# Performance work log

Measured on AMD Instinct MI355X. Metric: run time of the kernel, lower is better.

The kernel has to match this reference:

```python
import jax, jax.numpy as jnp
import numpy as np

DIM = 512
HEADS = 8
HEAD_DIM = DIM // HEADS
FFN = 1536
WIN = 16
EPS = 1e-6


def rms_norm(x, w):
    var = jnp.mean(x * x, axis=-1, keepdims=True)
    return x * jax.lax.rsqrt(var + EPS) * w


def rotate_half(x):
    x1, x2 = jnp.split(x, 2, axis=-1)
    return jnp.concatenate([-x2, x1], axis=-1)


def apply_rope(q, k, inv_freq, position_ids):
    # q,k: [B,H,S,D]; inv_freq: [D//2]; position_ids: [B,S]
    ang = position_ids[:, :, None].astype(jnp.float32) * inv_freq[None, None, :]  # [B,S,D/2]
    cos = jnp.concatenate([jnp.cos(ang), jnp.cos(ang)], axis=-1)[:, None]  # [B,1,S,D]
    sin = jnp.concatenate([jnp.sin(ang), jnp.sin(ang)], axis=-1)[:, None]
    q = q * cos + rotate_half(q) * sin
    k = k * cos + rotate_half(k) * sin
    return q, k


def setup_inputs() -> dict:
    key = jax.random.key(0)
    ks = jax.random.split(key, 12)
    B, S = 2, 4096
    x = jax.random.normal(ks[0], (B, S, DIM), dtype=jnp.float32)
    inv_freq = 1.0 / (10000.0 ** (jnp.arange(0, HEAD_DIM, 2, dtype=jnp.float32) / HEAD_DIM))  # [D/2]
    position_ids = jnp.broadcast_to(jnp.arange(S, dtype=jnp.int64), (B, S))
    key_padding_mask = jnp.zeros((B, S), dtype=bool)  # True = padded (ignored)
    s = 0.02
    return {
        "x": x,
        "rope_freqs": inv_freq,
        "position_ids": position_ids,
        "key_padding_mask": key_padding_mask,
        "norm1_w": jnp.ones((DIM,), jnp.float32),
        "wq": jax.random.normal(ks[1], (DIM, DIM), jnp.float32) * s,
        "wk": jax.random.normal(ks[2], (DIM, DIM), jnp.float32) * s,
        "wv": jax.random.normal(ks[3], (DIM, DIM), jnp.float32) * s,
        "wo": jax.random.normal(ks[4], (DIM, DIM), jnp.float32) * s,
        "norm2_w": jnp.ones((DIM,), jnp.float32),
        "w1": jax.random.normal(ks[5], (DIM, FFN), jnp.float32) * s,  # gate proj
        "w2": jax.random.normal(ks[6], (DIM, FFN), jnp.float32) * s,  # up proj
        "w3": jax.random.normal(ks[7], (FFN, DIM), jnp.float32) * s,  # down proj
    }


def local_attention(h, rope_freqs, position_ids, key_padding_mask, wq, wk, wv, wo):
    B, S, _ = h.shape
    q = jnp.einsum("bsd,de->bse", h, wq).reshape(B, S, HEADS, HEAD_DIM).transpose(0, 2, 1, 3)
    k = jnp.einsum("bsd,de->bse", h, wk).reshape(B, S, HEADS, HEAD_DIM).transpose(0, 2, 1, 3)
    v = jnp.einsum("bsd,de->bse", h, wv).reshape(B, S, HEADS, HEAD_DIM).transpose(0, 2, 1, 3)
    q, k = apply_rope(q, k, rope_freqs, position_ids)

    offs = jnp.arange(-WIN, WIN + 1)                       # [W]
    pos = jnp.arange(S)[:, None] + offs[None, :]           # [S,W]
    in_range = (pos >= 0) & (pos < S)                      # [S,W]
    pos_c = jnp.clip(pos, 0, S - 1)
    k_band = k[:, :, pos_c]                                # [B,H,S,W,D]
    v_band = v[:, :, pos_c]
    scores = jnp.einsum("bhsd,bhswd->bhsw", q, k_band) * (HEAD_DIM ** -0.5)
    keep = in_range[None, None] & (~key_padding_mask[:, pos_c])[:, None]  # [B,1->H,S,W]
    scores = jnp.where(keep, scores, -1e9)
    attn = jax.nn.softmax(scores, axis=-1)
    out = jnp.einsum("bhsw,bhswd->bhsd", attn, v_band)
    out = out.transpose(0, 2, 1, 3).reshape(B, S, DIM)
    return jnp.einsum("bsd,de->bse", out, wo)


def swiglu(h, w1, w2, w3):
    return jnp.einsum("bsf,fd->bsd", jax.nn.silu(h @ w1) * (h @ w2), w3)


def reference(x, rope_freqs, position_ids, key_padding_mask,
              norm1_w, wq, wk, wv, wo, norm2_w, w1, w2, w3):
    x = x + local_attention(rms_norm(x, norm1_w), rope_freqs, position_ids,
                            key_padding_mask, wq, wk, wv, wo)
    x = x + swiglu(rms_norm(x, norm2_w), w1, w2, w3)
    return x
```

## Files before the change

kernel.cpp:

```cpp
#include <hip/hip_runtime.h>
#include <math.h>

#define DIM   512
#define HEADS 8
#define HD    64
#define FFN_N 1536
#define WIN   16
#define SEQ   4096
#define BAND  (64 + 2 * WIN)
#define LDH   72

#define QKVN  1536

typedef __attribute__((ext_vector_type(8))) short bf16x8;
typedef __attribute__((ext_vector_type(4))) float f32x4;
typedef _Float16 f16;
typedef __attribute__((ext_vector_type(2))) _Float16 f16x2;

__device__ inline unsigned short f2bf(float f) {
  union { float f; unsigned u; } v; v.f = f;
  unsigned r = (v.u + 0x7FFF + ((v.u >> 16) & 1)) >> 16;
  return (unsigned short)r;
}

__device__ __forceinline__ float fast_rcp(float x) {
#if __has_builtin(__builtin_amdgcn_rcpf)
  return __builtin_amdgcn_rcpf(x);
#else
  return 1.0f / x;
#endif
}

__device__ __forceinline__ void gl2lds16(const void* g, void* l) {
  __builtin_amdgcn_global_load_lds(
      (const __attribute__((address_space(1))) unsigned int*)g,
      (__attribute__((address_space(3))) unsigned int*)l, 16, 0, 0);
}

__global__ __launch_bounds__(256) void k_preamble(
    const float* __restrict__ wq, const float* __restrict__ wk, const float* __restrict__ wv,
    const float* __restrict__ wo, const float* __restrict__ w1, const float* __restrict__ w2,
    const float* __restrict__ w3,
    unsigned short* __restrict__ BTqkv, unsigned short* __restrict__ BTwo,
    unsigned short* __restrict__ BTw12, unsigned short* __restrict__ BTw3,
    const float* __restrict__ invf, float* __restrict__ Ct, float* __restrict__ St,
    const float* __restrict__ X, const float* __restrict__ n1w,
    unsigned short* __restrict__ H, int ntok) {
  int bid = blockIdx.x;
  if (bid < 3328) {
    const float* src; unsigned short* dst; int K, N, t;
    if      (bid < 256)  { src = wq; dst = BTqkv;               K = 512;  N = 512;  t = bid; }
    else if (bid < 512)  { src = wk; dst = BTqkv + 512 * 512;   K = 512;  N = 512;  t = bid - 256; }
    else if (bid < 768)  { src = wv; dst = BTqkv + 1024 * 512;  K = 512;  N = 512;  t = bid - 512; }
    else if (bid < 1024) { src = wo; dst = BTwo;                K = 512;  N = 512;  t = bid - 768; }
    else if (bid < 1792) { src = w1; dst = BTw12;               K = 512;  N = 1536; t = bid - 1024; }
    else if (bid < 2560) { src = w2; dst = BTw12 + 1536 * 512;  K = 512;  N = 1536; t = bid - 1792; }
    else                 { src = w3; dst = BTw3;                K = 1536; N = 512;  t = bid - 2560; }
    int ntn = N >> 5;
    int tn = t % ntn, tk = t / ntn;
    __shared__ float T[32][33];
    int r = threadIdx.x >> 3, c = (threadIdx.x & 7) << 2;
    float4 s = *(const float4*)(src + (size_t)(tk * 32 + r) * N + tn * 32 + c);
    T[r][c + 0] = s.x; T[r][c + 1] = s.y; T[r][c + 2] = s.z; T[r][c + 3] = s.w;
    __syncthreads();
    ushort4 o = make_ushort4(f2bf(T[c + 0][r]), f2bf(T[c + 1][r]), f2bf(T[c + 2][r]), f2bf(T[c + 3][r]));
    *(ushort4*)(dst + (size_t)(tn * 32 + r) * K + tk * 32 + c) = o;
  } else if (bid < 3840) {
    int idx = (bid - 3328) * 256 + threadIdx.x;
    int p = idx & 31;
    int s = idx >> 5;
    float ang = (float)s * invf[p];
    float sn, cs;
    __sincosf(ang, &sn, &cs);
    Ct[idx] = cs;
    St[idx] = sn;
  } else {
    int wave = (bid - 3840) * 4 + (threadIdx.x >> 6);
    if (wave >= ntok) return;
    int lane = threadIdx.x & 63;
    const float* x = X + (size_t)wave * DIM;
    float4 a = *(const float4*)(x + lane * 4);
    float4 b = *(const float4*)(x + 256 + lane * 4);
    float ss = a.x*a.x + a.y*a.y + a.z*a.z + a.w*a.w
             + b.x*b.x + b.y*b.y + b.z*b.z + b.w*b.w;
#pragma unroll
    for (int off = 32; off; off >>= 1) ss += __shfl_xor(ss, off, 64);
    float r = rsqrtf(ss * (1.0f / DIM) + 1e-6f);
    float4 wa = *(const float4*)(n1w + lane * 4);
    float4 wb = *(const float4*)(n1w + 256 + lane * 4);
    unsigned short* o = H + (size_t)wave * DIM;
    *(ushort4*)(o + lane * 4)       = make_ushort4(f2bf(a.x*r*wa.x), f2bf(a.y*r*wa.y), f2bf(a.z*r*wa.z), f2bf(a.w*r*wa.w));
    *(ushort4*)(o + 256 + lane * 4) = make_ushort4(f2bf(b.x*r*wb.x), f2bf(b.y*r*wb.y), f2bf(b.z*r*wb.z), f2bf(b.w*r*wb.w));
  }
}

__global__ __launch_bounds__(256) void k_rmsnorm(const float* __restrict__ X,
                                                 const float* __restrict__ W,
                                                 unsigned short* __restrict__ O, int ntok) {
  int wave = blockIdx.x * 4 + (threadIdx.x >> 6);
  if (wave >= ntok) return;
  int lane = threadIdx.x & 63;
  const float* x = X + (size_t)wave * DIM;
  float4 a = *(const float4*)(x + lane * 4);
  float4 b = *(const float4*)(x + 256 + lane * 4);
  float ss = a.x*a.x + a.y*a.y + a.z*a.z + a.w*a.w
           + b.x*b.x + b.y*b.y + b.z*b.z + b.w*b.w;
#pragma unroll
  for (int off = 32; off; off >>= 1) ss += __shfl_xor(ss, off, 64);
  float r = rsqrtf(ss * (1.0f / DIM) + 1e-6f);
  float4 wa = *(const float4*)(W + lane * 4);
  float4 wb = *(const float4*)(W + 256 + lane * 4);
  unsigned short* o = O + (size_t)wave * DIM;
  *(ushort4*)(o + lane * 4)       = make_ushort4(f2bf(a.x*r*wa.x), f2bf(a.y*r*wa.y), f2bf(a.z*r*wa.z), f2bf(a.w*r*wa.w));
  *(ushort4*)(o + 256 + lane * 4) = make_ushort4(f2bf(b.x*r*wb.x), f2bf(b.y*r*wb.y), f2bf(b.z*r*wb.z), f2bf(b.w*r*wb.w));
}

__global__ __launch_bounds__(256) void k_mgemm(
    const unsigned short* __restrict__ A, const unsigned short* __restrict__ BT,
    float* __restrict__ C, const float* __restrict__ R, int M, int N, int K) {
  __shared__ __align__(16) unsigned short As[128 * 32];
  __shared__ __align__(16) unsigned short Bs[64 * 32];
  int tid = threadIdx.x;
  int lane = tid & 63, wave = tid >> 6;
  int q4 = lane >> 4, l16 = lane & 15;
  int bN = blockIdx.x, bM = blockIdx.y;

  f32x4 acc[2][4];
#pragma unroll
  for (int i = 0; i < 2; ++i)
#pragma unroll
    for (int j = 0; j < 4; ++j) acc[i][j] = (f32x4){0.f, 0.f, 0.f, 0.f};

  int lrow = lane >> 2;
  int cg   = (((lane & 3) ^ ((lane >> 3) & 3)) << 3);
  unsigned short* AsW0 = As + (wave * 32) * 32;
  unsigned short* AsW1 = As + (wave * 32 + 16) * 32;
  unsigned short* BsW  = Bs + (wave * 16) * 32;
  const unsigned short* Ag0 = A  + (size_t)(bM * 128 + wave * 32 + lrow) * K + cg;
  const unsigned short* Ag1 = Ag0 + (size_t)16 * K;
  const unsigned short* Bg  = BT + (size_t)(bN * 64 + wave * 16 + lrow) * K + cg;

  int xc = ((q4 ^ ((l16 >> 1) & 3)) << 3);

  for (int k0 = 0; k0 < K; k0 += 32) {
    __syncthreads();
    gl2lds16(Ag0 + k0, AsW0);
    gl2lds16(Ag1 + k0, AsW1);
    gl2lds16(Bg  + k0, BsW);
    __syncthreads();
    bf16x8 af[2], bf[4];
#pragma unroll
    for (int mi = 0; mi < 2; ++mi)
      af[mi] = *(const bf16x8*)&As[(wave * 32 + mi * 16 + l16) * 32 + xc];
#pragma unroll
    for (int ni = 0; ni < 4; ++ni)
      bf[ni] = *(const bf16x8*)&Bs[(ni * 16 + l16) * 32 + xc];
#pragma unroll
    for (int mi = 0; mi < 2; ++mi)
#pragma unroll
      for (int ni = 0; ni < 4; ++ni)
        acc[mi][ni] = __builtin_amdgcn_mfma_f32_16x16x32_bf16(af[mi], bf[ni], acc[mi][ni], 0, 0, 0);
  }
#pragma unroll
  for (int mi = 0; mi < 2; ++mi)
#pragma unroll
    for (int ni = 0; ni < 4; ++ni) {
      int col = bN * 64 + ni * 16 + l16;
#pragma unroll
      for (int r = 0; r < 4; ++r) {
        int row = bM * 128 + wave * 32 + mi * 16 + q4 * 4 + r;
        float v = acc[mi][ni][r];
        if (R) v += R[(size_t)row * N + col];
        C[(size_t)row * N + col] = v;
      }
    }
}

__global__ __launch_bounds__(256) void k_mgemm128(
    const unsigned short* __restrict__ A, const unsigned short* __restrict__ BT,
    float* __restrict__ C, int M, int N, int K) {
  __shared__ __align__(16) unsigned short As[128 * 32];
  __shared__ __align__(16) unsigned short Bs[128 * 32];
  int tid = threadIdx.x;
  int lane = tid & 63, wave = tid >> 6;
  int wm = wave & 1, wn = wave >> 1;
  int q4 = lane >> 4, l16 = lane & 15;
  int bN = blockIdx.x, bM = blockIdx.y;

  f32x4 acc[4][4];
#pragma unroll
  for (int i = 0; i < 4; ++i)
#pragma unroll
    for (int j = 0; j < 4; ++j) acc[i][j] = (f32x4){0.f, 0.f, 0.f, 0.f};

  int lrow = lane >> 2;
  int cg   = (((lane & 3) ^ ((lane >> 3) & 3)) << 3);
  unsigned short* AsW0 = As + (wave * 32) * 32;
  unsigned short* AsW1 = As + (wave * 32 + 16) * 32;
  unsigned short* BsW0 = Bs + (wave * 32) * 32;
  unsigned short* BsW1 = Bs + (wave * 32 + 16) * 32;
  const unsigned short* Ag0 = A  + (size_t)(bM * 128 + wave * 32 + lrow) * K + cg;
  const unsigned short* Ag1 = Ag0 + (size_t)16 * K;
  const unsigned short* Bg0 = BT + (size_t)(bN * 128 + wave * 32 + lrow) * K + cg;
  const unsigned short* Bg1 = Bg0 + (size_t)16 * K;

  int xc = ((q4 ^ ((l16 >> 1) & 3)) << 3);

  for (int k0 = 0; k0 < K; k0 += 32) {
    __syncthreads();
    gl2lds16(Ag0 + k0, AsW0);
    gl2lds16(Ag1 + k0, AsW1);
    gl2lds16(Bg0 + k0, BsW0);
    gl2lds16(Bg1 + k0, BsW1);
    __syncthreads();
    bf16x8 af[4], bf[4];
#pragma unroll
    for (int mi = 0; mi < 4; ++mi)
      af[mi] = *(const bf16x8*)&As[(wm * 64 + mi * 16 + l16) * 32 + xc];
#pragma unroll
    for (int ni = 0; ni < 4; ++ni)
      bf[ni] = *(const bf16x8*)&Bs[(wn * 64 + ni * 16 + l16) * 32 + xc];
#pragma unroll
    for (int mi = 0; mi < 4; ++mi)
#pragma unroll
      for (int ni = 0; ni < 4; ++ni)
        acc[mi][ni] = __builtin_amdgcn_mfma_f32_16x16x32_bf16(af[mi], bf[ni], acc[mi][ni], 0, 0, 0);
  }
#pragma unroll
  for (int mi = 0; mi < 4; ++mi)
#pragma unroll
    for (int ni = 0; ni < 4; ++ni) {
      int col = bN * 128 + wn * 64 + ni * 16 + l16;
#pragma unroll
      for (int r = 0; r < 4; ++r) {
        int row = bM * 128 + wm * 64 + mi * 16 + q4 * 4 + r;
        C[(size_t)row * N + col] = acc[mi][ni][r];
      }
    }
}

__global__ __launch_bounds__(256) void k_mgemm_swiglu(
    const unsigned short* __restrict__ A, const unsigned short* __restrict__ B1T,
    const unsigned short* __restrict__ B2T, unsigned short* __restrict__ Y,
    int M, int N, int K) {
  __shared__ __align__(16) unsigned short As[128 * 32];
  __shared__ __align__(16) unsigned short B1s[64 * 32];
  __shared__ __align__(16) unsigned short B2s[64 * 32];
  int tid = threadIdx.x;
  int lane = tid & 63, wave = tid >> 6;
  int q4 = lane >> 4, l16 = lane & 15;
  int bN = blockIdx.x, bM = blockIdx.y;

  f32x4 acc[2][2][4];
#pragma unroll
  for (int t = 0; t < 2; ++t)
#pragma unroll
    for (int i = 0; i < 2; ++i)
#pragma unroll
      for (int j = 0; j < 4; ++j) acc[t][i][j] = (f32x4){0.f, 0.f, 0.f, 0.f};

  int lrow = lane >> 2;
  int cg   = (((lane & 3) ^ ((lane >> 3) & 3)) << 3);
  unsigned short* AsW0 = As  + (wave * 32) * 32;
  unsigned short* AsW1 = As  + (wave * 32 + 16) * 32;
  unsigned short* B1sW = B1s + (wave * 16) * 32;
  unsigned short* B2sW = B2s + (wave * 16) * 32;
  const unsigned short* Ag0 = A   + (size_t)(bM * 128 + wave * 32 + lrow) * K + cg;
  const unsigned short* Ag1 = Ag0 + (size_t)16 * K;
  const unsigned short* B1g = B1T + (size_t)(bN * 64 + wave * 16 + lrow) * K + cg;
  const unsigned short* B2g = B2T + (size_t)(bN * 64 + wave * 16 + lrow) * K + cg;

  int xc = ((q4 ^ ((l16 >> 1) & 3)) << 3);

  for (int k0 = 0; k0 < K; k0 += 32) {
    __syncthreads();
    gl2lds16(Ag0 + k0, AsW0);
    gl2lds16(Ag1 + k0, AsW1);
    gl2lds16(B1g + k0, B1sW);
    gl2lds16(B2g + k0, B2sW);
    __syncthreads();
    bf16x8 af[2], b1f[4], b2f[4];
#pragma unroll
    for (int mi = 0; mi < 2; ++mi)
      af[mi] = *(const bf16x8*)&As[(wave * 32 + mi * 16 + l16) * 32 + xc];
#pragma unroll
    for (int ni = 0; ni < 4; ++ni) {
      b1f[ni] = *(const bf16x8*)&B1s[(ni * 16 + l16) * 32 + xc];
      b2f[ni] = *(const bf16x8*)&B2s[(ni * 16 + l16) * 32 + xc];
    }
#pragma unroll
    for (int mi = 0; mi < 2; ++mi)
#pragma unroll
      for (int ni = 0; ni < 4; ++ni) {
        acc[0][mi][ni] = __builtin_amdgcn_mfma_f32_16x16x32_bf16(af[mi], b1f[ni], acc[0][mi][ni], 0, 0, 0);
        acc[1][mi][ni] = __builtin_amdgcn_mfma_f32_16x16x32_bf16(af[mi], b2f[ni], acc[1][mi][ni], 0, 0, 0);
      }
  }
#pragma unroll
  for (int mi = 0; mi < 2; ++mi)
#pragma unroll
    for (int ni = 0; ni < 4; ++ni) {
      int col = bN * 64 + ni * 16 + l16;
#pragma unroll
      for (int r = 0; r < 4; ++r) {
        int row = bM * 128 + wave * 32 + mi * 16 + q4 * 4 + r;
        float g = acc[0][mi][ni][r];
        float u = acc[1][mi][ni][r];
        float yv = g * fast_rcp(1.0f + __expf(-g)) * u;
        Y[(size_t)row * N + col] = f2bf(yv);
      }
    }
}

__global__ __launch_bounds__(128) void k_attn(const float* __restrict__ QKV,
                                              const float* __restrict__ Ct,
                                              const float* __restrict__ St,
                                              unsigned short* __restrict__ O) {
  __shared__ __align__(16) unsigned short KV[BAND * LDH];
  int tid = threadIdx.x;
  int c0 = blockIdx.x * 64;
  int h = blockIdx.y, b = blockIdx.z;

#pragma unroll
  for (int base = 0; base < BAND; base += 16) {
    int r  = base + (tid >> 3);
    int c8 = (tid & 7) << 3;
    int sr = c0 - WIN + r;
    int scl = min(max(sr, 0), SEQ - 1);
    const float* kr = QKV + ((size_t)(b * SEQ + scl)) * QKVN + h * HD + 512;
    int p = c8 & 31;
    float4 v0 = *(const float4*)(kr + c8);
    float4 v1 = *(const float4*)(kr + c8 + 4);
    float4 u0 = *(const float4*)(kr + (c8 ^ 32));
    float4 u1 = *(const float4*)(kr + (c8 ^ 32) + 4);
    float4 cv0 = *(const float4*)(Ct + scl * 32 + p);
    float4 cv1 = *(const float4*)(Ct + scl * 32 + p + 4);
    float4 sv0 = *(const float4*)(St + scl * 32 + p);
    float4 sv1 = *(const float4*)(St + scl * 32 + p + 4);
    float sg = (c8 < 32) ? -1.f : 1.f;
    union { int4 w; f16 x[8]; } pk;
    pk.x[0] = (f16)(v0.x * cv0.x + sg * u0.x * sv0.x);
    pk.x[1] = (f16)(v0.y * cv0.y + sg * u0.y * sv0.y);
    pk.x[2] = (f16)(v0.z * cv0.z + sg * u0.z * sv0.z);
    pk.x[3] = (f16)(v0.w * cv0.w + sg * u0.w * sv0.w);
    pk.x[4] = (f16)(v1.x * cv1.x + sg * u1.x * sv1.x);
    pk.x[5] = (f16)(v1.y * cv1.y + sg * u1.y * sv1.y);
    pk.x[6] = (f16)(v1.z * cv1.z + sg * u1.z * sv1.z);
    pk.x[7] = (f16)(v1.w * cv1.w + sg * u1.w * sv1.w);
    *(int4*)&KV[r * LDH + c8] = pk.w;
  }
  __syncthreads();

  int lane = tid & 63;
  int ql   = (tid >> 6) * 32 + (lane >> 1);
  int half = lane & 1;
  int s    = c0 + ql;

  const float* qp = QKV + ((size_t)(b * SEQ + s)) * QKVN + h * HD;
  f16x2 qh[16];
  {
    float sg = half ? 1.f : -1.f;
#pragma unroll
    for (int i = 0; i < 8; ++i) {
      float4 ow = *(const float4*)(qp + half * 32 + 4 * i);
      float4 pr = *(const float4*)(qp + (half ^ 1) * 32 + 4 * i);
      float4 cv = *(const float4*)(Ct + (size_t)s * 32 + 4 * i);
      float4 sv = *(const float4*)(St + (size_t)s * 32 + 4 * i);
      float r0f = ow.x * cv.x + sg * pr.x * sv.x;
      float r1f = ow.y * cv.y + sg * pr.y * sv.y;
      float r2f = ow.z * cv.z + sg * pr.z * sv.z;
      float r3f = ow.w * cv.w + sg * pr.w * sv.w;
      qh[2 * i]     = (f16x2){(f16)r0f, (f16)r1f};
      qh[2 * i + 1] = (f16x2){(f16)r2f, (f16)r3f};
    }
  }

  int jlo = max(s - WIN, 0);
  int nj  = min(s + WIN, SEQ - 1) - jlo + 1;
  int r0  = jlo - (c0 - WIN);

  float sc[33];
#pragma unroll
  for (int t = 0; t < 33; ++t) {
    const unsigned short* kr = &KV[(r0 + t) * LDH + half * 32];
    union { int4 w; f16x2 hx[4]; } L[4];
    L[0].w = *(const int4*)(kr);
    L[1].w = *(const int4*)(kr + 8);
    L[2].w = *(const int4*)(kr + 16);
    L[3].w = *(const int4*)(kr + 24);
    float pa = 0.f, pb = 0.f;
#pragma unroll
    for (int k = 0; k < 4; ++k) {
#if __has_builtin(__builtin_amdgcn_fdot2)
      pa = __builtin_amdgcn_fdot2(qh[4 * k + 0], L[k].hx[0], pa, false);
      pb = __builtin_amdgcn_fdot2(qh[4 * k + 1], L[k].hx[1], pb, false);
      pa = __builtin_amdgcn_fdot2(qh[4 * k + 2], L[k].hx[2], pa, false);
      pb = __builtin_amdgcn_fdot2(qh[4 * k + 3], L[k].hx[3], pb, false);
#else
#pragma unroll
      for (int j = 0; j < 4; ++j) {
        pa += (float)qh[4 * k + j][0] * (float)L[k].hx[j][0];
        pb += (float)qh[4 * k + j][1] * (float)L[k].hx[j][1];
      }
#endif
    }
    float sv = pa + pb;
    sv += __shfl_xor(sv, 1, 64);
    sc[t] = (t < nj) ? sv * 0.125f : -1e30f;
  }
  float m = -1e30f;
#pragma unroll
  for (int t = 0; t < 33; ++t) m = fmaxf(m, sc[t]);
  float sum = 0.f;
#pragma unroll
  for (int t = 0; t < 33; ++t) { float e = __expf(sc[t] - m); sc[t] = e; sum += e; }
  float inv = fast_rcp(sum);

  __syncthreads();

#pragma unroll
  for (int base = 0; base < BAND; base += 16) {
    int r  = base + (tid >> 3);
    int c8 = (tid & 7) << 3;
    int sr = c0 - WIN + r;
    int scl = min(max(sr, 0), SEQ - 1);
    const float* vr = QKV + ((size_t)(b * SEQ + scl)) * QKVN + h * HD + 1024;
    float4 v0 = *(const float4*)(vr + c8);
    float4 v1 = *(const float4*)(vr + c8 + 4);
    union { int4 w; f16 x[8]; } pk;
    pk.x[0] = (f16)v0.x; pk.x[1] = (f16)v0.y; pk.x[2] = (f16)v0.z; pk.x[3] = (f16)v0.w;
    pk.x[4] = (f16)v1.x; pk.x[5] = (f16)v1.y; pk.x[6] = (f16)v1.z; pk.x[7] = (f16)v1.w;
    *(int4*)&KV[r * LDH + c8] = pk.w;
  }
  __syncthreads();

  float o[32];
#pragma unroll
  for (int i = 0; i < 32; ++i) o[i] = 0.f;
#pragma unroll
  for (int t = 0; t < 33; ++t) {
    float w = sc[t] * inv;
    const unsigned short* vr = &KV[(r0 + t) * LDH + half * 32];
    union { int4 w4; f16 x[8]; } A[4];
    A[0].w4 = *(const int4*)(vr);
    A[1].w4 = *(const int4*)(vr + 8);
    A[2].w4 = *(const int4*)(vr + 16);
    A[3].w4 = *(const int4*)(vr + 24);
#pragma unroll
    for (int k = 0; k < 4; ++k)
#pragma unroll
      for (int j = 0; j < 8; ++j)
        o[8 * k + j] += w * (float)A[k].x[j];
  }
  unsigned short* op = O + ((size_t)(b * SEQ + s)) * DIM + h * HD + half * 32;
#pragma unroll
  for (int v = 0; v < 4; ++v) {
    union { int4 w; unsigned short u[8]; } pk;
#pragma unroll
    for (int j = 0; j < 8; ++j) pk.u[j] = f2bf(o[8 * v + j]);
    *(int4*)(op + 8 * v) = pk.w;
  }
}

extern "C" void kernel_launch(void* const* d_in, const int* in_sizes, int n_in,
                              void* d_out, int out_size, void* d_ws, size_t ws_size,
                              hipStream_t stream) {
  const float* x    = (const float*)d_in[0];
  const float* invf = (const float*)d_in[1];
  const float* n1w = (const float*)d_in[4];
  const float* wq  = (const float*)d_in[5];
  const float* wk  = (const float*)d_in[6];
  const float* wv  = (const float*)d_in[7];
  const float* wo  = (const float*)d_in[8];
  const float* n2w = (const float*)d_in[9];
  const float* w1  = (const float*)d_in[10];
  const float* w2  = (const float*)d_in[11];
  const float* w3  = (const float*)d_in[12];
  float* out = (float*)d_out;

  const int ntok = in_sizes[0] / DIM;
  const int B    = ntok / SEQ;

  unsigned char* p = (unsigned char*)d_ws;
  float* QKV = (float*)p;                    p += (size_t)ntok * QKVN * 4;
  unsigned short* hbf  = (unsigned short*)p; p += (size_t)ntok * DIM * 2;
  unsigned short* aO   = (unsigned short*)p; p += (size_t)ntok * DIM * 2;
  unsigned short* h2   = (unsigned short*)p; p += (size_t)ntok * DIM * 2;
  unsigned short* yb   = (unsigned short*)p; p += (size_t)ntok * FFN_N * 2;
  unsigned short* BTqkv= (unsigned short*)p; p += (size_t)QKVN * DIM * 2;
  unsigned short* BTwo = (unsigned short*)p; p += (size_t)DIM * DIM * 2;
  unsigned short* BTw12= (unsigned short*)p; p += (size_t)2 * FFN_N * DIM * 2;
  unsigned short* BTw3 = (unsigned short*)p; p += (size_t)DIM * FFN_N * 2;
  float* Ct = (float*)p;                     p += (size_t)SEQ * 32 * 4;
  float* St = (float*)p;                     p += (size_t)SEQ * 32 * 4;

  k_preamble<<<3328 + 512 + ntok / 4, 256, 0, stream>>>(
      wq, wk, wv, wo, w1, w2, w3, BTqkv, BTwo, BTw12, BTw3,
      invf, Ct, St, x, n1w, hbf, ntok);
  {
    dim3 g(QKVN / 128, ntok / 128);
    k_mgemm128<<<g, 256, 0, stream>>>(hbf, BTqkv, QKV, ntok, QKVN, DIM);
  }
  {
    dim3 gA(SEQ / 64, HEADS, B);
    k_attn<<<gA, 128, 0, stream>>>(QKV, Ct, St, aO);
  }
  {
    dim3 g(DIM / 64, ntok / 128);
    k_mgemm<<<g, 256, 0, stream>>>(aO, BTwo, out, x, ntok, DIM, DIM);
  }
  k_rmsnorm<<<ntok / 4, 256, 0, stream>>>(out, n2w, h2, ntok);
  {
    dim3 g(FFN_N / 64, ntok / 128);
    k_mgemm_swiglu<<<g, 256, 0, stream>>>(h2, BTw12, BTw12 + (size_t)FFN_N * DIM, yb, ntok, FFN_N, DIM);
  }
  {
    dim3 g(DIM / 64, ntok / 128);
    k_mgemm<<<g, 256, 0, stream>>>(yb, BTw3, out, out, ntok, DIM, FFN_N);
  }
}
```

Before: 255.5 us.

## Store QKV projection as fp16 and XOR-swizzle attention LDS tiles

The QKV GEMM now writes fp16 instead of fp32, which halves the intermediate buffer's write and read traffic. The attention kernel loads fp16 K/V/Q with single int4 loads, applies RoPE in float, and copies V straight into shared memory without converting it. The padded LDS row stride is replaced by an unpadded layout with an XOR swizzle to avoid bank conflicts. Rounding Q/K to fp16 before RoPE adds a small precision loss, and fp16 range could overflow for large projections.

Result: faster. 246.8 us (-3.4%).

```diff
diff --git a/kernel.cpp b/kernel.cpp
--- a/kernel.cpp
+++ b/kernel.cpp
@@ -8,7 +8,7 @@
 #define WIN   16
 #define SEQ   4096
 #define BAND  (64 + 2 * WIN)
-#define LDH   72
+#define LDA   64
 
 #define QKVN  1536
 
@@ -178,7 +178,7 @@
 
 __global__ __launch_bounds__(256) void k_mgemm128(
     const unsigned short* __restrict__ A, const unsigned short* __restrict__ BT,
-    float* __restrict__ C, int M, int N, int K) {
+    f16* __restrict__ C, int M, int N, int K) {
   __shared__ __align__(16) unsigned short As[128 * 32];
   __shared__ __align__(16) unsigned short Bs[128 * 32];
   int tid = threadIdx.x;
@@ -234,7 +234,7 @@
 #pragma unroll
       for (int r = 0; r < 4; ++r) {
         int row = bM * 128 + wm * 64 + mi * 16 + q4 * 4 + r;
-        C[(size_t)row * N + col] = acc[mi][ni][r];
+        C[(size_t)row * N + col] = (f16)acc[mi][ni][r];
       }
     }
 }
@@ -312,11 +312,11 @@
     }
 }
 
-__global__ __launch_bounds__(128) void k_attn(const float* __restrict__ QKV,
+__global__ __launch_bounds__(128) void k_attn(const f16* __restrict__ QKV,
                                               const float* __restrict__ Ct,
                                               const float* __restrict__ St,
                                               unsigned short* __restrict__ O) {
-  __shared__ __align__(16) unsigned short KV[BAND * LDH];
+  __shared__ __align__(16) f16 KV[BAND * LDA];
   int tid = threadIdx.x;
   int c0 = blockIdx.x * 64;
   int h = blockIdx.y, b = blockIdx.z;
@@ -327,27 +327,22 @@
     int c8 = (tid & 7) << 3;
     int sr = c0 - WIN + r;
     int scl = min(max(sr, 0), SEQ - 1);
-    const float* kr = QKV + ((size_t)(b * SEQ + scl)) * QKVN + h * HD + 512;
+    const f16* kr = QKV + ((size_t)(b * SEQ + scl)) * QKVN + h * HD + 512;
     int p = c8 & 31;
-    float4 v0 = *(const float4*)(kr + c8);
-    float4 v1 = *(const float4*)(kr + c8 + 4);
-    float4 u0 = *(const float4*)(kr + (c8 ^ 32));
-    float4 u1 = *(const float4*)(kr + (c8 ^ 32) + 4);
+    union { int4 w; f16 x[8]; } ov, pv, pk;
+    ov.w = *(const int4*)(kr + c8);
+    pv.w = *(const int4*)(kr + (c8 ^ 32));
     float4 cv0 = *(const float4*)(Ct + scl * 32 + p);
     float4 cv1 = *(const float4*)(Ct + scl * 32 + p + 4);
     float4 sv0 = *(const float4*)(St + scl * 32 + p);
     float4 sv1 = *(const float4*)(St + scl * 32 + p + 4);
+    float cs[8] = {cv0.x, cv0.y, cv0.z, cv0.w, cv1.x, cv1.y, cv1.z, cv1.w};
+    float sn[8] = {sv0.x, sv0.y, sv0.z, sv0.w, sv1.x, sv1.y, sv1.z, sv1.w};
     float sg = (c8 < 32) ? -1.f : 1.f;
-    union { int4 w; f16 x[8]; } pk;
-    pk.x[0] = (f16)(v0.x * cv0.x + sg * u0.x * sv0.x);
-    pk.x[1] = (f16)(v0.y * cv0.y + sg * u0.y * sv0.y);
-    pk.x[2] = (f16)(v0.z * cv0.z + sg * u0.z * sv0.z);
-    pk.x[3] = (f16)(v0.w * cv0.w + sg * u0.w * sv0.w);
-    pk.x[4] = (f16)(v1.x * cv1.x + sg * u1.x * sv1.x);
-    pk.x[5] = (f16)(v1.y * cv1.y + sg * u1.y * sv1.y);
-    pk.x[6] = (f16)(v1.z * cv1.z + sg * u1.z * sv1.z);
-    pk.x[7] = (f16)(v1.w * cv1.w + sg * u1.w * sv1.w);
-    *(int4*)&KV[r * LDH + c8] = pk.w;
+#pragma unroll
+    for (int j = 0; j < 8; ++j)
+      pk.x[j] = (f16)((float)ov.x[j] * cs[j] + sg * (float)pv.x[j] * sn[j]);
+    *(int4*)&KV[r * LDA + ((((c8 >> 3) ^ (r & 7))) << 3)] = pk.w;
   }
   __syncthreads();
 
@@ -356,22 +351,27 @@
   int half = lane & 1;
   int s    = c0 + ql;
 
-  const float* qp = QKV + ((size_t)(b * SEQ + s)) * QKVN + h * HD;
+  const f16* qp = QKV + ((size_t)(b * SEQ + s)) * QKVN + h * HD;
   f16x2 qh[16];
   {
     float sg = half ? 1.f : -1.f;
 #pragma unroll
-    for (int i = 0; i < 8; ++i) {
-      float4 ow = *(const float4*)(qp + half * 32 + 4 * i);
-      float4 pr = *(const float4*)(qp + (half ^ 1) * 32 + 4 * i);
-      float4 cv = *(const float4*)(Ct + (size_t)s * 32 + 4 * i);
-      float4 sv = *(const float4*)(St + (size_t)s * 32 + 4 * i);
-      float r0f = ow.x * cv.x + sg * pr.x * sv.x;
-      float r1f = ow.y * cv.y + sg * pr.y * sv.y;
-      float r2f = ow.z * cv.z + sg * pr.z * sv.z;
-      float r3f = ow.w * cv.w + sg * pr.w * sv.w;
-      qh[2 * i]     = (f16x2){(f16)r0f, (f16)r1f};
-      qh[2 * i + 1] = (f16x2){(f16)r2f, (f16)r3f};
+    for (int k = 0; k < 4; ++k) {
+      union { int4 w; f16 x[8]; } ov, pv;
+      ov.w = *(const int4*)(qp + half * 32 + 8 * k);
+      pv.w = *(const int4*)(qp + (half ^ 1) * 32 + 8 * k);
+      float4 cv0 = *(const float4*)(Ct + (size_t)s * 32 + 8 * k);
+      float4 cv1 = *(const float4*)(Ct + (size_t)s * 32 + 8 * k + 4);
+      float4 sv0 = *(const float4*)(St + (size_t)s * 32 + 8 * k);
+      float4 sv1 = *(const float4*)(St + (size_t)s * 32 + 8 * k + 4);
+      float cs[8] = {cv0.x, cv0.y, cv0.z, cv0.w, cv1.x, cv1.y, cv1.z, cv1.w};
+      float sn[8] = {sv0.x, sv0.y, sv0.z, sv0.w, sv1.x, sv1.y, sv1.z, sv1.w};
+#pragma unroll
+      for (int j = 0; j < 4; ++j) {
+        float a = (float)ov.x[2 * j]     * cs[2 * j]     + sg * (float)pv.x[2 * j]     * sn[2 * j];
+        float c = (float)ov.x[2 * j + 1] * cs[2 * j + 1] + sg * (float)pv.x[2 * j + 1] * sn[2 * j + 1];
+        qh[4 * k + j] = (f16x2){(f16)a, (f16)c};
+      }
     }
   }
 
@@ -382,12 +382,13 @@
   float sc[33];
 #pragma unroll
   for (int t = 0; t < 33; ++t) {
-    const unsigned short* kr = &KV[(r0 + t) * LDH + half * 32];
+    int rr = r0 + t;
+    const f16* kr = &KV[rr * LDA];
+    int sw = rr & 7;
     union { int4 w; f16x2 hx[4]; } L[4];
-    L[0].w = *(const int4*)(kr);
-    L[1].w = *(const int4*)(kr + 8);
-    L[2].w = *(const int4*)(kr + 16);
-    L[3].w = *(const int4*)(kr + 24);
+#pragma unroll
+    for (int jj = 0; jj < 4; ++jj)
+      L[jj].w = *(const int4*)(kr + (((half * 4 + jj) ^ sw) << 3));
     float pa = 0.f, pb = 0.f;
 #pragma unroll
     for (int k = 0; k < 4; ++k) {
@@ -424,13 +425,9 @@
     int c8 = (tid & 7) << 3;
     int sr = c0 - WIN + r;
     int scl = min(max(sr, 0), SEQ - 1);
-    const float* vr = QKV + ((size_t)(b * SEQ + scl)) * QKVN + h * HD + 1024;
-    float4 v0 = *(const float4*)(vr + c8);
-    float4 v1 = *(const float4*)(vr + c8 + 4);
-    union { int4 w; f16 x[8]; } pk;
-    pk.x[0] = (f16)v0.x; pk.x[1] = (f16)v0.y; pk.x[2] = (f16)v0.z; pk.x[3] = (f16)v0.w;
-    pk.x[4] = (f16)v1.x; pk.x[5] = (f16)v1.y; pk.x[6] = (f16)v1.z; pk.x[7] = (f16)v1.w;
-    *(int4*)&KV[r * LDH + c8] = pk.w;
+    const f16* vr = QKV + ((size_t)(b * SEQ + scl)) * QKVN + h * HD + 1024;
+    int4 w = *(const int4*)(vr + c8);
+    *(int4*)&KV[r * LDA + ((((c8 >> 3) ^ (r & 7))) << 3)] = w;
   }
   __syncthreads();
 
@@ -440,12 +437,13 @@
 #pragma unroll
   for (int t = 0; t < 33; ++t) {
     float w = sc[t] * inv;
-    const unsigned short* vr = &KV[(r0 + t) * LDH + half * 32];
+    int rr = r0 + t;
+    const f16* vr = &KV[rr * LDA];
+    int sw = rr & 7;
     union { int4 w4; f16 x[8]; } A[4];
-    A[0].w4 = *(const int4*)(vr);
-    A[1].w4 = *(const int4*)(vr + 8);
-    A[2].w4 = *(const int4*)(vr + 16);
-    A[3].w4 = *(const int4*)(vr + 24);
+#pragma unroll
+    for (int jj = 0; jj < 4; ++jj)
+      A[jj].w4 = *(const int4*)(vr + (((half * 4 + jj) ^ sw) << 3));
 #pragma unroll
     for (int k = 0; k < 4; ++k)
 #pragma unroll
@@ -482,7 +480,7 @@
   const int B    = ntok / SEQ;
 
   unsigned char* p = (unsigned char*)d_ws;
-  float* QKV = (float*)p;                    p += (size_t)ntok * QKVN * 4;
+  f16* QKV = (f16*)p;                        p += (size_t)ntok * QKVN * 2;
   unsigned short* hbf  = (unsigned short*)p; p += (size_t)ntok * DIM * 2;
   unsigned short* aO   = (unsigned short*)p; p += (size_t)ntok * DIM * 2;
   unsigned short* h2   = (unsigned short*)p; p += (size_t)ntok * DIM * 2;
```
